# Kernel tuning notes

Measured on AMD Instinct MI355X. Metric: run time of the kernel, lower is better.

The kernel has to match this reference:

```python
import jax, jax.numpy as jnp
import numpy as np

DIM, HID = 1024, 2048
N_SHARED, N_ROUTED, TOP_K = 2, 6, 2
AUX_W = 0.01
B, T = 4, 2048


def _swiglu(x, w1, w2, w3):
    # x: [N, C]; w1,w3: [C, H]; w2: [H, C]
    return (jax.nn.silu(x @ w1) * (x @ w3)) @ w2


def setup_inputs() -> dict:
    key = jax.random.key(0)
    ks = jax.random.split(key, 9)
    s = 0.02
    return {
        "x": jax.random.normal(ks[0], (B, T, DIM), dtype=jnp.float32),
        "w1_s": jax.random.normal(ks[1], (N_SHARED, DIM, HID), dtype=jnp.float32) * s,
        "w2_s": jax.random.normal(ks[2], (N_SHARED, HID, DIM), dtype=jnp.float32) * s,
        "w3_s": jax.random.normal(ks[3], (N_SHARED, DIM, HID), dtype=jnp.float32) * s,
        "w1_r": jax.random.normal(ks[4], (N_ROUTED, DIM, HID), dtype=jnp.float32) * s,
        "w2_r": jax.random.normal(ks[5], (N_ROUTED, HID, DIM), dtype=jnp.float32) * s,
        "w3_r": jax.random.normal(ks[6], (N_ROUTED, DIM, HID), dtype=jnp.float32) * s,
        "gate_w": jax.random.normal(ks[7], (DIM, N_ROUTED), dtype=jnp.float32) * s,
        "out_w": jax.random.normal(ks[8], (DIM, DIM), dtype=jnp.float32) * s,
    }


def reference(x, w1_s, w2_s, w3_s, w1_r, w2_r, w3_r, gate_w, out_w):
    Bv, Tv, C = x.shape
    xf = x.reshape(-1, C)  # [N, C]

    # shared experts: always run for every token
    shared = jnp.zeros_like(xf)
    for e in range(N_SHARED):
        shared = shared + _swiglu(xf, w1_s[e], w2_s[e], w3_s[e])

    # router
    logits = xf @ gate_w                       # [N, E]
    wk, idx = jax.lax.top_k(logits, TOP_K)     # [N, K]
    wk = jax.nn.softmax(wk, axis=-1)           # softmax over selected k only

    # routed experts: dense per-expert pass scaled by (zero for unselected) weight
    routed = jnp.zeros_like(xf)
    for e in range(N_ROUTED):
        we = jnp.sum(wk * (idx == e).astype(xf.dtype), axis=-1, keepdims=True)  # [N,1]
        routed = routed + we * _swiglu(xf, w1_r[e], w2_r[e], w3_r[e])

    combined = shared + routed

    # aux load-balance loss (top-1 assignment fraction x mean prob)
    probs = jax.nn.softmax(logits, axis=-1)
    f_i = jnp.mean(jax.nn.one_hot(idx[:, 0], N_ROUTED, dtype=xf.dtype), axis=0)
    p_i = jnp.mean(probs, axis=0)
    aux_loss = AUX_W * N_ROUTED * jnp.sum(f_i * p_i)

    out = (combined @ out_w).reshape(Bv, Tv, C)
    return out, aux_loss
```

## Files before the change

### kernel.cpp

```cpp
#include <hip/hip_runtime.h>
#include <hip/hip_bf16.h>
#include <cstdint>

#define DIMc 1024
#define HIDc 2048
#define NTOK 8192
#define NRT 6

typedef __bf16 bf16x8 __attribute__((ext_vector_type(8)));
typedef __bf16 bf16x4 __attribute__((ext_vector_type(4)));
typedef __bf16 bf16x2v __attribute__((ext_vector_type(2)));
typedef float  f32x4  __attribute__((ext_vector_type(4)));

#define VMCNT(n) asm volatile("s_waitcnt vmcnt(" #n ")" ::: "memory")
#define RBAR()   asm volatile("s_barrier" ::: "memory")

__device__ __forceinline__ void gl_lds16(const void* gsrc, void* ldst) {
    auto g = (const __attribute__((address_space(1))) void*)gsrc;
    auto l = (__attribute__((address_space(3))) void*)ldst;
    __builtin_amdgcn_global_load_lds(g, l, 16, 0, 0);
}

__device__ __forceinline__ void xcd_swz(int lid, int nwg, int gx, int& bx, int& by) {
    int q = nwg >> 3, r = nwg & 7;
    int xcd = lid & 7, idx = lid >> 3;
    int nlid = (xcd < r ? xcd * (q + 1) : r * (q + 1) + (xcd - r) * q) + idx;
    bx = nlid % gx; by = nlid / gx;
}

__global__ __launch_bounds__(256) void tcvt_k(
    const float* __restrict__ w1s, const float* __restrict__ w2s, const float* __restrict__ w3s,
    const float* __restrict__ w1r, const float* __restrict__ w2r, const float* __restrict__ w3r,
    const float* __restrict__ outw,
    __bf16* __restrict__ W13T, __bf16* __restrict__ W2T, __bf16* __restrict__ OutWT)
{
    int id = blockIdx.z;
    const float* src; __bf16* dst; int K, N;
    if (id < 16) {
        int ex = id >> 1, half = id & 1;
        const float* w1 = (ex < 2) ? w1s + (size_t)ex * DIMc * HIDc : w1r + (size_t)(ex - 2) * DIMc * HIDc;
        const float* w3 = (ex < 2) ? w3s + (size_t)ex * DIMc * HIDc : w3r + (size_t)(ex - 2) * DIMc * HIDc;
        src = half ? w3 : w1;
        K = 1024; N = 2048;
        dst = W13T + (size_t)ex * 4096 * 1024 + (size_t)half * 2048 * 1024;
    } else if (id < 24) {
        int ex = id - 16;
        src = (ex < 2) ? w2s + (size_t)ex * HIDc * DIMc : w2r + (size_t)(ex - 2) * HIDc * DIMc;
        K = 2048; N = 1024;
        dst = W2T + (size_t)ex * 2048 * 1024;
    } else {
        src = outw; K = 1024; N = 1024; dst = OutWT;
    }
    int n0 = blockIdx.x * 32, k0 = blockIdx.y * 32;
    if (n0 >= N || k0 >= K) return;
    __shared__ float t[32][33];
    int c = threadIdx.x & 31, rb = threadIdx.x >> 5;
#pragma unroll
    for (int i = 0; i < 4; i++) {
        int r = rb + i * 8;
        t[r][c] = src[(size_t)(k0 + r) * N + n0 + c];
    }
    __syncthreads();
    int kp = threadIdx.x & 15, nn = threadIdx.x >> 4;
#pragma unroll
    for (int pass = 0; pass < 2; pass++) {
        int n = nn + pass * 16;
        bf16x2v v; v[0] = (__bf16)t[2 * kp][n]; v[1] = (__bf16)t[2 * kp + 1][n];
        *(bf16x2v*)&dst[(size_t)(n0 + n) * K + k0 + 2 * kp] = v;
    }
}

__global__ __launch_bounds__(256) void router_k(
    const float* __restrict__ x, const float* __restrict__ gate,
    __bf16* __restrict__ xb, int* __restrict__ tke, float* __restrict__ tkw,
    float* __restrict__ auxp, float* __restrict__ auxf, int* __restrict__ rcnt)
{
    __shared__ float gl[DIMc * NRT];
    __shared__ float pacc[NRT];
    __shared__ int hist1[NRT], hist2[NRT];
    for (int i = threadIdx.x; i < DIMc * NRT; i += 256) gl[i] = gate[i];
    if (threadIdx.x < NRT) { pacc[threadIdx.x] = 0.f; hist1[threadIdx.x] = 0; hist2[threadIdx.x] = 0; }
    __syncthreads();
    int lane = threadIdx.x & 63, wid = threadIdx.x >> 6;
    for (int rep = 0; rep < 4; rep++) {
        int t = blockIdx.x * 16 + wid * 4 + rep;
        float a[NRT] = {0.f, 0.f, 0.f, 0.f, 0.f, 0.f};
        const float* xr = x + (size_t)t * DIMc;
        __bf16* xbr = xb + (size_t)t * DIMc;
        for (int k = lane; k < DIMc; k += 64) {
            float v = xr[k];
            xbr[k] = (__bf16)v;
#pragma unroll
            for (int e = 0; e < NRT; e++) a[e] += v * gl[k * NRT + e];
        }
#pragma unroll
        for (int e = 0; e < NRT; e++)
#pragma unroll
            for (int m = 32; m; m >>= 1) a[e] += __shfl_xor(a[e], m);
        if (lane == 0) {
            int i0 = 0; float m0 = a[0];
#pragma unroll
            for (int e = 1; e < NRT; e++) if (a[e] > m0) { m0 = a[e]; i0 = e; }
            int i1 = -1; float m1 = -1e30f;
#pragma unroll
            for (int e = 0; e < NRT; e++) if (e != i0 && a[e] > m1) { m1 = a[e]; i1 = e; }
            float w1 = __expf(m1 - m0);
            float inv = 1.f / (1.f + w1);
            tke[2 * t] = i0; tke[2 * t + 1] = i1;
            tkw[2 * t] = inv; tkw[2 * t + 1] = w1 * inv;
            float se = 0.f, pe[NRT];
#pragma unroll
            for (int e = 0; e < NRT; e++) { pe[e] = __expf(a[e] - m0); se += pe[e]; }
            float rinv = 1.f / se;
#pragma unroll
            for (int e = 0; e < NRT; e++) atomicAdd(&pacc[e], pe[e] * rinv);
            atomicAdd(&hist1[i0], 1);
            atomicAdd(&hist2[i0], 1); atomicAdd(&hist2[i1], 1);
        }
    }
    __syncthreads();
    if (threadIdx.x < NRT) {
        atomicAdd(&auxp[threadIdx.x], pacc[threadIdx.x]);
        atomicAdd(&auxf[threadIdx.x], (float)hist1[threadIdx.x]);
        atomicAdd(&rcnt[threadIdx.x], hist2[threadIdx.x]);
    }
}

__global__ void offsets_k(const int* __restrict__ rcnt, int* __restrict__ goff, int* __restrict__ gcnt) {
    if (threadIdx.x == 0) {
        goff[0] = 0; goff[1] = NTOK; gcnt[0] = NTOK; gcnt[1] = NTOK;
        int off = 0;
        for (int e = 0; e < NRT; e++) { goff[2 + e] = off; gcnt[2 + e] = rcnt[e]; off += rcnt[e]; }
    }
}

__global__ __launch_bounds__(256) void scatter_k(
    const int* __restrict__ tke, const float* __restrict__ tkw,
    const int* __restrict__ goff, int* __restrict__ curs,
    int* __restrict__ perm, float* __restrict__ wrow)
{
    int t = blockIdx.x * 256 + threadIdx.x;
    if (t >= NTOK) return;
    perm[t] = t;        wrow[t] = 1.f;
    perm[NTOK + t] = t; wrow[NTOK + t] = 1.f;
#pragma unroll
    for (int k = 0; k < 2; k++) {
        int e = tke[2 * t + k]; float w = tkw[2 * t + k];
        int slot = atomicAdd(&curs[e], 1);
        int pos = 2 * NTOK + goff[2 + e] + slot;
        perm[pos] = t; wrow[pos] = w;
    }
}

__global__ void auxfin_k(const float* __restrict__ auxp, const float* __restrict__ auxf, float* __restrict__ out) {
    if (threadIdx.x == 0) {
        float s = 0.f;
        for (int e = 0; e < NRT; e++) s += (auxf[e] * (1.f / NTOK)) * (auxp[e] * (1.f / NTOK));
        out[(size_t)NTOK * DIMc] = 0.01f * 6.f * s;
    }
}

__global__ __launch_bounds__(512, 2) void gemm13_k(
    const __bf16* __restrict__ A, const __bf16* __restrict__ Bbase, __bf16* __restrict__ outB,
    const int* __restrict__ goff, const int* __restrict__ gcnt, const int* __restrict__ perm,
    int gbase, int pbase)
{
    __shared__ __bf16 lds[2 * 32768];
    const int g = gbase + blockIdx.z;
    const int cnt = gcnt[g];
    int bx, by;
    xcd_swz(blockIdx.x + gridDim.x * blockIdx.y, gridDim.x * gridDim.y, gridDim.x, bx, by);
    if (bx * 256 >= cnt) return;
    const int gofs = goff[g];
    const int tid = threadIdx.x;
    const int lane = tid & 63, wid = tid >> 6;
    const int wr = wid >> 1, wc = wid & 1;
    const int l15 = lane & 15, l4 = lane >> 4;

    const __bf16* Bg = Bbase + (size_t)g * (4096 * 1024);

    const __bf16* agA[4]; const __bf16* agB1[2]; const __bf16* agB3[2];
    int ldsA[4], ldsB[2];
#pragma unroll
    for (int i = 0; i < 4; i++) {
        int chunk = i * 512 + tid;
        int row = chunk >> 3, cg = (chunk & 7) ^ (row & 7);
        int r = bx * 256 + row; if (r > cnt - 1) r = cnt - 1;
        agA[i] = A + (size_t)perm[pbase + gofs + r] * 1024 + cg * 8;
        ldsA[i] = chunk * 8;
    }
#pragma unroll
    for (int i = 0; i < 2; i++) {
        int chunk = i * 512 + tid;
        int row = chunk >> 3, cg = (chunk & 7) ^ (row & 7);
        int nr = by * 128 + row;
        agB1[i] = Bg + (size_t)nr * 1024 + cg * 8;
        agB3[i] = Bg + (size_t)(2048 + nr) * 1024 + cg * 8;
        ldsB[i] = chunk * 8;
    }

#define STAGE13(b, kt) { __bf16* d_ = lds + (b) * 32768; \
    _Pragma("unroll") for (int i_ = 0; i_ < 4; i_++) gl_lds16(agA[i_] + (kt) * 64, d_ + ldsA[i_]); \
    _Pragma("unroll") for (int i_ = 0; i_ < 2; i_++) { \
        gl_lds16(agB1[i_] + (kt) * 64, d_ + 16384 + ldsB[i_]); \
        gl_lds16(agB3[i_] + (kt) * 64, d_ + 24576 + ldsB[i_]); } }

    f32x4 acc1[4][4], acc3[4][4];
#pragma unroll
    for (int mi = 0; mi < 4; mi++)
#pragma unroll
        for (int ni = 0; ni < 4; ni++)
#pragma unroll
            for (int j = 0; j < 4; j++) { acc1[mi][ni][j] = 0.f; acc3[mi][ni][j] = 0.f; }

    const int nkt = 16;
    STAGE13(0, 0);
    for (int kt = 0; kt < nkt; kt++) {
        const int cur = kt & 1;
        if (kt + 1 < nkt) { STAGE13(cur ^ 1, kt + 1); VMCNT(8); }
        else              { VMCNT(0); }
        RBAR();
        const __bf16* As  = lds + cur * 32768;
        const __bf16* B1s = As + 16384;
        const __bf16* B3s = As + 24576;
#pragma unroll
        for (int kk = 0; kk < 64; kk += 32) {
            bf16x8 av[4];
#pragma unroll
            for (int mi = 0; mi < 4; mi++) {
                int lr = wr * 64 + mi * 16 + l15;
                int cr = ((kk >> 3) + l4) ^ (lr & 7);
                av[mi] = *(const bf16x8*)&As[lr * 64 + cr * 8];
            }
#pragma unroll
            for (int ni = 0; ni < 4; ni++) {
                int lr = wc * 64 + ni * 16 + l15;
                int cr = ((kk >> 3) + l4) ^ (lr & 7);
                bf16x8 bv1 = *(const bf16x8*)&B1s[lr * 64 + cr * 8];
                bf16x8 bv3 = *(const bf16x8*)&B3s[lr * 64 + cr * 8];
#pragma unroll
                for (int mi = 0; mi < 4; mi++) {
                    acc1[mi][ni] = __builtin_amdgcn_mfma_f32_16x16x32_bf16(av[mi], bv1, acc1[mi][ni], 0, 0, 0);
                    acc3[mi][ni] = __builtin_amdgcn_mfma_f32_16x16x32_bf16(av[mi], bv3, acc3[mi][ni], 0, 0, 0);
                }
            }
        }
        RBAR();
    }

#pragma unroll
    for (int mi = 0; mi < 4; mi++) {
#pragma unroll
        for (int j = 0; j < 4; j++) {
            int r = bx * 256 + wr * 64 + mi * 16 + l4 * 4 + j;
            if (r < cnt) {
                size_t orow = (size_t)(gofs + r) * 2048;
#pragma unroll
                for (int ni = 0; ni < 4; ni++) {
                    int c = by * 128 + wc * 64 + ni * 16 + l15;
                    float h1 = acc1[mi][ni][j], h3 = acc3[mi][ni][j];
                    float sg = h1 / (1.f + __expf(-h1));
                    outB[orow + c] = (__bf16)(sg * h3);
                }
            }
        }
    }
#undef STAGE13
}

template <int MODE>
__global__ __launch_bounds__(256, 2) void gemmNN_k(
    const __bf16* __restrict__ A, const __bf16* __restrict__ Bbase,
    float* __restrict__ outF,
    const int* __restrict__ goff, const int* __restrict__ gcnt,
    const int* __restrict__ perm, const float* __restrict__ wrow,
    int gbase, int pbase, int K)
{
    __shared__ __bf16 lds[2 * 16384];
    const int g = gbase + blockIdx.z;
    const int cnt = gcnt[g];
    int bx, by;
    xcd_swz(blockIdx.x + gridDim.x * blockIdx.y, gridDim.x * gridDim.y, gridDim.x, bx, by);
    if (bx * 128 >= cnt) return;
    const int gofs = goff[g];
    const int tid = threadIdx.x;
    const int lane = tid & 63, wid = tid >> 6;
    const int wr = wid >> 1, wc = wid & 1;
    const int l15 = lane & 15, l4 = lane >> 4;

    const __bf16* Bg = (MODE == 1) ? Bbase + (size_t)g * (2048 * 1024) : Bbase;

    const __bf16* agA[4]; const __bf16* agB[4];
    int ldsOf[4];
#pragma unroll
    for (int i = 0; i < 4; i++) {
        int chunk = i * 256 + tid;
        int row = chunk >> 3, cg = (chunk & 7) ^ (row & 7);
        int r = bx * 128 + row; if (r > cnt - 1) r = cnt - 1;
        size_t arow = (MODE == 1) ? (size_t)(gofs + r) : (size_t)r;
        agA[i] = A + arow * (size_t)K + cg * 8;
        agB[i] = Bg + (size_t)(by * 128 + row) * K + cg * 8;
        ldsOf[i] = chunk * 8;
    }

#define STAGENN(b, kt) { __bf16* d_ = lds + (b) * 16384; \
    _Pragma("unroll") for (int i_ = 0; i_ < 4; i_++) { \
        gl_lds16(agA[i_] + (kt) * 64, d_ + ldsOf[i_]); \
        gl_lds16(agB[i_] + (kt) * 64, d_ + 8192 + ldsOf[i_]); } }

    f32x4 acc[4][4];
#pragma unroll
    for (int mi = 0; mi < 4; mi++)
#pragma unroll
        for (int ni = 0; ni < 4; ni++)
#pragma unroll
            for (int j = 0; j < 4; j++) acc[mi][ni][j] = 0.f;

    const int nkt = K >> 6;
    STAGENN(0, 0);
    for (int kt = 0; kt < nkt; kt++) {
        const int cur = kt & 1;
        if (kt + 1 < nkt) { STAGENN(cur ^ 1, kt + 1); VMCNT(8); }
        else              { VMCNT(0); }
        RBAR();
        const __bf16* As = lds + cur * 16384;
        const __bf16* Bs = As + 8192;
#pragma unroll
        for (int kk = 0; kk < 64; kk += 32) {
            bf16x8 av[4];
#pragma unroll
            for (int mi = 0; mi < 4; mi++) {
                int lr = wr * 64 + mi * 16 + l15;
                int cr = ((kk >> 3) + l4) ^ (lr & 7);
                av[mi] = *(const bf16x8*)&As[lr * 64 + cr * 8];
            }
#pragma unroll
            for (int ni = 0; ni < 4; ni++) {
                int lr = wc * 64 + ni * 16 + l15;
                int cr = ((kk >> 3) + l4) ^ (lr & 7);
                bf16x8 bv = *(const bf16x8*)&Bs[lr * 64 + cr * 8];
#pragma unroll
                for (int mi = 0; mi < 4; mi++)
                    acc[mi][ni] = __builtin_amdgcn_mfma_f32_16x16x32_bf16(av[mi], bv, acc[mi][ni], 0, 0, 0);
            }
        }
        RBAR();
    }

#pragma unroll
    for (int mi = 0; mi < 4; mi++) {
#pragma unroll
        for (int j = 0; j < 4; j++) {
            int r = bx * 128 + wr * 64 + mi * 16 + l4 * 4 + j;
            if (r < cnt) {
                if constexpr (MODE == 1) {
                    int pos = pbase + gofs + r;
                    int tok = perm[pos]; float w = wrow[pos];
                    size_t orow = (size_t)tok * 1024;
#pragma unroll
                    for (int ni = 0; ni < 4; ni++) {
                        int c = by * 128 + wc * 64 + ni * 16 + l15;
                        atomicAdd(&outF[orow + c], w * acc[mi][ni][j]);
                    }
                } else {
                    size_t orow = (size_t)r * 1024;
#pragma unroll
                    for (int ni = 0; ni < 4; ni++) {
                        int c = by * 128 + wc * 64 + ni * 16 + l15;
                        outF[orow + c] = acc[mi][ni][j];
                    }
                }
            }
        }
    }
#undef STAGENN
}

__global__ __launch_bounds__(256) void cvtcomb_k(const float* __restrict__ c, __bf16* __restrict__ cb) {
    size_t i = (size_t)blockIdx.x * 256 + threadIdx.x;
    const float4* s = (const float4*)c;
    float4 v = s[i];
    bf16x4 o; o[0] = (__bf16)v.x; o[1] = (__bf16)v.y; o[2] = (__bf16)v.z; o[3] = (__bf16)v.w;
    ((bf16x4*)cb)[i] = o;
}

extern "C" void kernel_launch(void* const* d_in, const int* in_sizes, int n_in,
                              void* d_out, int out_size, void* d_ws, size_t ws_size,
                              hipStream_t stream) {
    const float* x    = (const float*)d_in[0];
    const float* w1s  = (const float*)d_in[1];
    const float* w2s  = (const float*)d_in[2];
    const float* w3s  = (const float*)d_in[3];
    const float* w1r  = (const float*)d_in[4];
    const float* w2r  = (const float*)d_in[5];
    const float* w3r  = (const float*)d_in[6];
    const float* gate = (const float*)d_in[7];
    const float* outw = (const float*)d_in[8];
    float* out = (float*)d_out;

    char* ws = (char*)d_ws;
    float* combined = (float*)ws;
    float* auxp = (float*)(ws + 33554432);
    float* auxf = auxp + 8;
    int*   rcnt = (int*)(ws + 33554432 + 64);
    int*   curs = rcnt + 8;
    size_t off = 33554432 + 256;
    __bf16* xb    = (__bf16*)(ws + off); off += 16777216;
    __bf16* W13T  = (__bf16*)(ws + off); off += 67108864;
    __bf16* W2T   = (__bf16*)(ws + off); off += 33554432;
    __bf16* OutWT = (__bf16*)(ws + off); off += 2097152;
    __bf16* gbuf  = (__bf16*)(ws + off); off += 67108864;
    __bf16* cb    = gbuf;
    int*   tke  = (int*)(ws + off);   off += 65536;
    float* tkw  = (float*)(ws + off); off += 65536;
    int*   perm = (int*)(ws + off);   off += 131072;
    float* wrow = (float*)(ws + off); off += 131072;
    int*   goffp = (int*)(ws + off);  off += 64;
    int*   gcntp = (int*)(ws + off);  off += 64;

    hipMemsetAsync(d_ws, 0, 33554432 + 256, stream);

    dim3 b256(256), b512(512);
    tcvt_k<<<dim3(64, 64, 25), b256, 0, stream>>>(w1s, w2s, w3s, w1r, w2r, w3r, outw, W13T, W2T, OutWT);
    router_k<<<dim3(512), b256, 0, stream>>>(x, gate, xb, tke, tkw, auxp, auxf, rcnt);
    offsets_k<<<dim3(1), dim3(64), 0, stream>>>(rcnt, goffp, gcntp);
    scatter_k<<<dim3(32), b256, 0, stream>>>(tke, tkw, goffp, curs, perm, wrow);
    auxfin_k<<<dim3(1), dim3(64), 0, stream>>>(auxp, auxf, out);

    gemm13_k<<<dim3(32, 16, 2), b512, 0, stream>>>(xb, W13T, gbuf, goffp, gcntp, perm, 0, 0);
    gemmNN_k<1><<<dim3(64, 8, 2), b256, 0, stream>>>(gbuf, W2T, combined, goffp, gcntp, perm, wrow, 0, 0, 2048);
    gemm13_k<<<dim3(32, 16, 6), b512, 0, stream>>>(xb, W13T, gbuf, goffp, gcntp, perm, 2, 2 * NTOK);
    gemmNN_k<1><<<dim3(64, 8, 6), b256, 0, stream>>>(gbuf, W2T, combined, goffp, gcntp, perm, wrow, 2, 2 * NTOK, 2048);

    cvtcomb_k<<<dim3(8192), b256, 0, stream>>>(combined, cb);
    gemmNN_k<2><<<dim3(64, 8, 1), b256, 0, stream>>>(cb, OutWT, out, goffp, gcntp, perm, wrow, 0, 0, 1024);
}
```

Measured before the change: 934.7 us.

## Merge shared experts into one wide GEMM and replace atomic scatter with gather-combine

The two shared experts are concatenated along the hidden dimension, so one gemm13 produces an 8192x4096 intermediate and one down-projection with K=4096 sums both experts in its accumulator. Routed down-projection outputs are written as weighted bf16 rows into a slot buffer instead of fp32 atomicAdd into a combined buffer. A new combine kernel gathers the shared row and the two routed slots per token into the bf16 input of the output GEMM. This removes float atomics, the 32MB memset and the fp32 conversion pass. In exchange it adds a 48MB bf16 intermediate and rounds partial sums to bf16 before they are added.

```diff
diff --git a/kernel.cpp b/kernel.cpp
--- a/kernel.cpp
+++ b/kernel.cpp
@@ -8,7 +8,6 @@
 #define NRT 6
 
 typedef __bf16 bf16x8 __attribute__((ext_vector_type(8)));
-typedef __bf16 bf16x4 __attribute__((ext_vector_type(4)));
 typedef __bf16 bf16x2v __attribute__((ext_vector_type(2)));
 typedef float  f32x4  __attribute__((ext_vector_type(4)));
 
@@ -35,21 +34,29 @@
     __bf16* __restrict__ W13T, __bf16* __restrict__ W2T, __bf16* __restrict__ OutWT)
 {
     int id = blockIdx.z;
-    const float* src; __bf16* dst; int K, N;
-    if (id < 16) {
-        int ex = id >> 1, half = id & 1;
-        const float* w1 = (ex < 2) ? w1s + (size_t)ex * DIMc * HIDc : w1r + (size_t)(ex - 2) * DIMc * HIDc;
-        const float* w3 = (ex < 2) ? w3s + (size_t)ex * DIMc * HIDc : w3r + (size_t)(ex - 2) * DIMc * HIDc;
-        src = half ? w3 : w1;
-        K = 1024; N = 2048;
-        dst = W13T + (size_t)ex * 4096 * 1024 + (size_t)half * 2048 * 1024;
+    const float* src; __bf16* dst; int K, N; size_t S;
+    if (id < 4) {
+        int half = id >> 1, ex = id & 1;
+        src = (half ? w3s : w1s) + (size_t)ex * DIMc * HIDc;
+        K = 1024; N = 2048; S = 1024;
+        dst = W13T + ((size_t)half * 4096 + ex * 2048) * 1024;
+    } else if (id < 16) {
+        int j = id - 4; int ex = j >> 1, half = j & 1;
+        src = (half ? w3r : w1r) + (size_t)ex * DIMc * HIDc;
+        K = 1024; N = 2048; S = 1024;
+        dst = W13T + ((size_t)8192 + ex * 4096 + half * 2048) * 1024;
+    } else if (id < 18) {
+        int ex = id - 16;
+        src = w2s + (size_t)ex * HIDc * DIMc;
+        K = 2048; N = 1024; S = 4096;
+        dst = W2T + ex * 2048;
     } else if (id < 24) {
-        int ex = id - 16;
-        src = (ex < 2) ? w2s + (size_t)ex * HIDc * DIMc : w2r + (size_t)(ex - 2) * HIDc * DIMc;
-        K = 2048; N = 1024;
-        dst = W2T + (size_t)ex * 2048 * 1024;
+        int ex = id - 18;
+        src = w2r + (size_t)ex * HIDc * DIMc;
+        K = 2048; N = 1024; S = 2048;
+        dst = W2T + (size_t)4096 * 1024 + (size_t)ex * 2048 * 1024;
     } else {
-        src = outw; K = 1024; N = 1024; dst = OutWT;
+        src = outw; K = 1024; N = 1024; S = 1024; dst = OutWT;
     }
     int n0 = blockIdx.x * 32, k0 = blockIdx.y * 32;
     if (n0 >= N || k0 >= K) return;
@@ -66,7 +73,7 @@
     for (int pass = 0; pass < 2; pass++) {
         int n = nn + pass * 16;
         bf16x2v v; v[0] = (__bf16)t[2 * kp][n]; v[1] = (__bf16)t[2 * kp + 1][n];
-        *(bf16x2v*)&dst[(size_t)(n0 + n) * K + k0 + 2 * kp] = v;
+        *(bf16x2v*)&dst[(size_t)(n0 + n) * S + k0 + 2 * kp] = v;
     }
 }
 
@@ -128,27 +135,24 @@
 
 __global__ void offsets_k(const int* __restrict__ rcnt, int* __restrict__ goff, int* __restrict__ gcnt) {
     if (threadIdx.x == 0) {
-        goff[0] = 0; goff[1] = NTOK; gcnt[0] = NTOK; gcnt[1] = NTOK;
         int off = 0;
-        for (int e = 0; e < NRT; e++) { goff[2 + e] = off; gcnt[2 + e] = rcnt[e]; off += rcnt[e]; }
+        for (int e = 0; e < NRT; e++) { goff[e] = off; gcnt[e] = rcnt[e]; off += rcnt[e]; }
     }
 }
 
 __global__ __launch_bounds__(256) void scatter_k(
     const int* __restrict__ tke, const float* __restrict__ tkw,
     const int* __restrict__ goff, int* __restrict__ curs,
-    int* __restrict__ perm, float* __restrict__ wrow)
+    int* __restrict__ perm, float* __restrict__ wrow, int* __restrict__ islot)
 {
     int t = blockIdx.x * 256 + threadIdx.x;
     if (t >= NTOK) return;
-    perm[t] = t;        wrow[t] = 1.f;
-    perm[NTOK + t] = t; wrow[NTOK + t] = 1.f;
 #pragma unroll
     for (int k = 0; k < 2; k++) {
         int e = tke[2 * t + k]; float w = tkw[2 * t + k];
         int slot = atomicAdd(&curs[e], 1);
-        int pos = 2 * NTOK + goff[2 + e] + slot;
-        perm[pos] = t; wrow[pos] = w;
+        int sr = goff[e] + slot;
+        perm[sr] = t; wrow[sr] = w; islot[2 * t + k] = sr;
     }
 }
 
@@ -160,25 +164,29 @@
     }
 }
 
+template <int SHARED>
 __global__ __launch_bounds__(512, 2) void gemm13_k(
-    const __bf16* __restrict__ A, const __bf16* __restrict__ Bbase, __bf16* __restrict__ outB,
-    const int* __restrict__ goff, const int* __restrict__ gcnt, const int* __restrict__ perm,
-    int gbase, int pbase)
+    const __bf16* __restrict__ A, const __bf16* __restrict__ W13, __bf16* __restrict__ gbuf,
+    const int* __restrict__ goff, const int* __restrict__ gcnt, const int* __restrict__ perm)
 {
     __shared__ __bf16 lds[2 * 32768];
-    const int g = gbase + blockIdx.z;
-    const int cnt = gcnt[g];
+    int cnt, gofs, h3ofs, gstride;
+    const __bf16* Bg;
+    if constexpr (SHARED) {
+        cnt = NTOK; gofs = 0; h3ofs = 4096 * 1024; gstride = 4096; Bg = W13;
+    } else {
+        int e = blockIdx.z;
+        cnt = gcnt[e]; gofs = goff[e]; h3ofs = 2048 * 1024; gstride = 2048;
+        Bg = W13 + ((size_t)8192 + (size_t)e * 4096) * 1024;
+    }
     int bx, by;
     xcd_swz(blockIdx.x + gridDim.x * blockIdx.y, gridDim.x * gridDim.y, gridDim.x, bx, by);
     if (bx * 256 >= cnt) return;
-    const int gofs = goff[g];
     const int tid = threadIdx.x;
     const int lane = tid & 63, wid = tid >> 6;
     const int wr = wid >> 1, wc = wid & 1;
     const int l15 = lane & 15, l4 = lane >> 4;
 
-    const __bf16* Bg = Bbase + (size_t)g * (4096 * 1024);
-
     const __bf16* agA[4]; const __bf16* agB1[2]; const __bf16* agB3[2];
     int ldsA[4], ldsB[2];
 #pragma unroll
@@ -186,7 +194,8 @@
         int chunk = i * 512 + tid;
         int row = chunk >> 3, cg = (chunk & 7) ^ (row & 7);
         int r = bx * 256 + row; if (r > cnt - 1) r = cnt - 1;
-        agA[i] = A + (size_t)perm[pbase + gofs + r] * 1024 + cg * 8;
+        size_t arow = SHARED ? (size_t)r : (size_t)perm[gofs + r];
+        agA[i] = A + arow * 1024 + cg * 8;
         ldsA[i] = chunk * 8;
     }
 #pragma unroll
@@ -195,7 +204,7 @@
         int row = chunk >> 3, cg = (chunk & 7) ^ (row & 7);
         int nr = by * 128 + row;
         agB1[i] = Bg + (size_t)nr * 1024 + cg * 8;
-        agB3[i] = Bg + (size_t)(2048 + nr) * 1024 + cg * 8;
+        agB3[i] = Bg + (size_t)h3ofs + (size_t)nr * 1024 + cg * 8;
         ldsB[i] = chunk * 8;
     }
 
@@ -254,13 +263,13 @@
         for (int j = 0; j < 4; j++) {
             int r = bx * 256 + wr * 64 + mi * 16 + l4 * 4 + j;
             if (r < cnt) {
-                size_t orow = (size_t)(gofs + r) * 2048;
+                size_t orow = (size_t)(gofs + r) * gstride;
 #pragma unroll
                 for (int ni = 0; ni < 4; ni++) {
                     int c = by * 128 + wc * 64 + ni * 16 + l15;
                     float h1 = acc1[mi][ni][j], h3 = acc3[mi][ni][j];
                     float sg = h1 / (1.f + __expf(-h1));
-                    outB[orow + c] = (__bf16)(sg * h3);
+                    gbuf[orow + c] = (__bf16)(sg * h3);
                 }
             }
         }
@@ -270,26 +279,29 @@
 
 template <int MODE>
 __global__ __launch_bounds__(256, 2) void gemmNN_k(
-    const __bf16* __restrict__ A, const __bf16* __restrict__ Bbase,
-    float* __restrict__ outF,
-    const int* __restrict__ goff, const int* __restrict__ gcnt,
-    const int* __restrict__ perm, const float* __restrict__ wrow,
-    int gbase, int pbase, int K)
+    const __bf16* __restrict__ A, const __bf16* __restrict__ B,
+    __bf16* __restrict__ outB16, float* __restrict__ outF32,
+    const float* __restrict__ wrow, const int* __restrict__ goff, const int* __restrict__ gcnt,
+    int K)
 {
     __shared__ __bf16 lds[2 * 16384];
-    const int g = gbase + blockIdx.z;
-    const int cnt = gcnt[g];
+    int cnt, gofs;
+    const __bf16* Bg;
+    if constexpr (MODE == 1) {
+        int e = blockIdx.z;
+        cnt = gcnt[e]; gofs = goff[e];
+        Bg = B + (size_t)e * 2048 * 1024;
+    } else {
+        cnt = NTOK; gofs = 0; Bg = B;
+    }
     int bx, by;
     xcd_swz(blockIdx.x + gridDim.x * blockIdx.y, gridDim.x * gridDim.y, gridDim.x, bx, by);
     if (bx * 128 >= cnt) return;
-    const int gofs = goff[g];
     const int tid = threadIdx.x;
     const int lane = tid & 63, wid = tid >> 6;
     const int wr = wid >> 1, wc = wid & 1;
     const int l15 = lane & 15, l4 = lane >> 4;
 
-    const __bf16* Bg = (MODE == 1) ? Bbase + (size_t)g * (2048 * 1024) : Bbase;
-
     const __bf16* agA[4]; const __bf16* agB[4];
     int ldsOf[4];
 #pragma unroll
@@ -297,8 +309,7 @@
         int chunk = i * 256 + tid;
         int row = chunk >> 3, cg = (chunk & 7) ^ (row & 7);
         int r = bx * 128 + row; if (r > cnt - 1) r = cnt - 1;
-        size_t arow = (MODE == 1) ? (size_t)(gofs + r) : (size_t)r;
-        agA[i] = A + arow * (size_t)K + cg * 8;
+        agA[i] = A + (size_t)(gofs + r) * K + cg * 8;
         agB[i] = Bg + (size_t)(by * 128 + row) * K + cg * 8;
         ldsOf[i] = chunk * 8;
     }
@@ -353,21 +364,28 @@
         for (int j = 0; j < 4; j++) {
             int r = bx * 128 + wr * 64 + mi * 16 + l4 * 4 + j;
             if (r < cnt) {
-                if constexpr (MODE == 1) {
-                    int pos = pbase + gofs + r;
-                    int tok = perm[pos]; float w = wrow[pos];
-                    size_t orow = (size_t)tok * 1024;
+                if constexpr (MODE == 0) {
+                    size_t orow = (size_t)r * 1024;
 #pragma unroll
                     for (int ni = 0; ni < 4; ni++) {
                         int c = by * 128 + wc * 64 + ni * 16 + l15;
-                        atomicAdd(&outF[orow + c], w * acc[mi][ni][j]);
+                        outB16[orow + c] = (__bf16)acc[mi][ni][j];
+                    }
+                } else if constexpr (MODE == 1) {
+                    int sr = gofs + r;
+                    float w = wrow[sr];
+                    size_t orow = (size_t)(8192 + sr) * 1024;
+#pragma unroll
+                    for (int ni = 0; ni < 4; ni++) {
+                        int c = by * 128 + wc * 64 + ni * 16 + l15;
+                        outB16[orow + c] = (__bf16)(w * acc[mi][ni][j]);
                     }
                 } else {
                     size_t orow = (size_t)r * 1024;
 #pragma unroll
                     for (int ni = 0; ni < 4; ni++) {
                         int c = by * 128 + wc * 64 + ni * 16 + l15;
-                        outF[orow + c] = acc[mi][ni][j];
+                        outF32[orow + c] = acc[mi][ni][j];
                     }
                 }
             }
@@ -376,12 +394,20 @@
 #undef STAGENN
 }
 
-__global__ __launch_bounds__(256) void cvtcomb_k(const float* __restrict__ c, __bf16* __restrict__ cb) {
-    size_t i = (size_t)blockIdx.x * 256 + threadIdx.x;
-    const float4* s = (const float4*)c;
-    float4 v = s[i];
-    bf16x4 o; o[0] = (__bf16)v.x; o[1] = (__bf16)v.y; o[2] = (__bf16)v.z; o[3] = (__bf16)v.w;
-    ((bf16x4*)cb)[i] = o;
+__global__ __launch_bounds__(256) void combine_k(
+    const __bf16* __restrict__ ybuf, const int* __restrict__ islot, __bf16* __restrict__ cb)
+{
+    int tid = threadIdx.x;
+    int row = blockIdx.x * 2 + (tid >> 7);
+    int c8 = (tid & 127) * 8;
+    int s0 = islot[2 * row], s1 = islot[2 * row + 1];
+    bf16x8 vs = *(const bf16x8*)&ybuf[(size_t)row * 1024 + c8];
+    bf16x8 v0 = *(const bf16x8*)&ybuf[(size_t)(8192 + s0) * 1024 + c8];
+    bf16x8 v1 = *(const bf16x8*)&ybuf[(size_t)(8192 + s1) * 1024 + c8];
+    bf16x8 o;
+#pragma unroll
+    for (int j = 0; j < 8; j++) o[j] = (__bf16)((float)vs[j] + (float)v0[j] + (float)v1[j]);
+    *(bf16x8*)&cb[(size_t)row * 1024 + c8] = o;
 }
 
 extern "C" void kernel_launch(void* const* d_in, const int* in_sizes, int n_in,
@@ -399,39 +425,40 @@
     float* out = (float*)d_out;
 
     char* ws = (char*)d_ws;
-    float* combined = (float*)ws;
-    float* auxp = (float*)(ws + 33554432);
+    float* auxp = (float*)ws;
     float* auxf = auxp + 8;
-    int*   rcnt = (int*)(ws + 33554432 + 64);
+    int*   rcnt = (int*)(ws + 64);
     int*   curs = rcnt + 8;
-    size_t off = 33554432 + 256;
+    size_t off = 256;
     __bf16* xb    = (__bf16*)(ws + off); off += 16777216;
     __bf16* W13T  = (__bf16*)(ws + off); off += 67108864;
     __bf16* W2T   = (__bf16*)(ws + off); off += 33554432;
     __bf16* OutWT = (__bf16*)(ws + off); off += 2097152;
     __bf16* gbuf  = (__bf16*)(ws + off); off += 67108864;
     __bf16* cb    = gbuf;
-    int*   tke  = (int*)(ws + off);   off += 65536;
-    float* tkw  = (float*)(ws + off); off += 65536;
-    int*   perm = (int*)(ws + off);   off += 131072;
-    float* wrow = (float*)(ws + off); off += 131072;
-    int*   goffp = (int*)(ws + off);  off += 64;
-    int*   gcntp = (int*)(ws + off);  off += 64;
-
-    hipMemsetAsync(d_ws, 0, 33554432 + 256, stream);
+    __bf16* ybuf  = (__bf16*)(ws + off); off += 50331648;
+    int*   tke   = (int*)(ws + off);   off += 65536;
+    float* tkw   = (float*)(ws + off); off += 65536;
+    int*   perm  = (int*)(ws + off);   off += 65536;
+    float* wrow  = (float*)(ws + off); off += 65536;
+    int*   islot = (int*)(ws + off);   off += 65536;
+    int*   goffp = (int*)(ws + off);   off += 64;
+    int*   gcntp = (int*)(ws + off);   off += 64;
+
+    hipMemsetAsync(d_ws, 0, 256, stream);
 
     dim3 b256(256), b512(512);
     tcvt_k<<<dim3(64, 64, 25), b256, 0, stream>>>(w1s, w2s, w3s, w1r, w2r, w3r, outw, W13T, W2T, OutWT);
     router_k<<<dim3(512), b256, 0, stream>>>(x, gate, xb, tke, tkw, auxp, auxf, rcnt);
     offsets_k<<<dim3(1), dim3(64), 0, stream>>>(rcnt, goffp, gcntp);
-    scatter_k<<<dim3(32), b256, 0, stream>>>(tke, tkw, goffp, curs, perm, wrow);
+    scatter_k<<<dim3(32), b256, 0, stream>>>(tke, tkw, goffp, curs, perm, wrow, islot);
     auxfin_k<<<dim3(1), dim3(64), 0, stream>>>(auxp, auxf, out);
 
-    gemm13_k<<<dim3(32, 16, 2), b512, 0, stream>>>(xb, W13T, gbuf, goffp, gcntp, perm, 0, 0);
-    gemmNN_k<1><<<dim3(64, 8, 2), b256, 0, stream>>>(gbuf, W2T, combined, goffp, gcntp, perm, wrow, 0, 0, 2048);
-    gemm13_k<<<dim3(32, 16, 6), b512, 0, stream>>>(xb, W13T, gbuf, goffp, gcntp, perm, 2, 2 * NTOK);
-    gemmNN_k<1><<<dim3(64, 8, 6), b256, 0, stream>>>(gbuf, W2T, combined, goffp, gcntp, perm, wrow, 2, 2 * NTOK, 2048);
-
-    cvtcomb_k<<<dim3(8192), b256, 0, stream>>>(combined, cb);
-    gemmNN_k<2><<<dim3(64, 8, 1), b256, 0, stream>>>(cb, OutWT, out, goffp, gcntp, perm, wrow, 0, 0, 1024);
-}
+    gemm13_k<1><<<dim3(32, 32, 1), b512, 0, stream>>>(xb, W13T, gbuf, goffp, gcntp, perm);
+    gemmNN_k<0><<<dim3(64, 8, 1), b256, 0, stream>>>(gbuf, W2T, ybuf, nullptr, wrow, goffp, gcntp, 4096);
+    gemm13_k<0><<<dim3(32, 16, 6), b512, 0, stream>>>(xb, W13T, gbuf, goffp, gcntp, perm);
+    gemmNN_k<1><<<dim3(64, 8, 6), b256, 0, stream>>>(gbuf, W2T + (size_t)4096 * 1024, ybuf, nullptr, wrow, goffp, gcntp, 2048);
+
+    combine_k<<<dim3(4096), b256, 0, stream>>>(ybuf, islot, cb);
+    gemmNN_k<2><<<dim3(64, 8, 1), b256, 0, stream>>>(cb, OutWT, nullptr, out, wrow, goffp, gcntp, 1024);
+}
```

Result: faster. 865.1 us (-7.4%).
